# Optimization experiments

Hardware: AMD Instinct MI355X
Metric: run time of the kernel (lower is better)

Reference implementation:

```python
import jax, jax.numpy as jnp
import numpy as np

K = 3
PAD = 1
KP = K * K


def setup_inputs() -> dict:
    key = jax.random.key(0)
    k1, k2, k3, k4 = jax.random.split(key, 4)
    B, C, O, H, W = 8, 64, 64, 128, 128
    x = jax.random.normal(k1, (B, C, H, W), dtype=jnp.float32)
    offset = jax.random.normal(k2, (B, 2 * KP, H, W), dtype=jnp.float32)
    weight = jax.random.normal(k3, (O, C, K, K), dtype=jnp.float32) * 0.05
    bias = jax.random.normal(k4, (O,), dtype=jnp.float32) * 0.05
    return {"x": x, "offset": offset, "weight": weight, "bias": bias}


def _deform_conv(x, offset, weight, bias):
    B, C, H, W = x.shape
    O = weight.shape[0]
    x_pad = jnp.pad(x, ((0, 0), (0, 0), (PAD, PAD), (PAD, PAD)))
    Hp, Wp = H + 2 * PAD, W + 2 * PAD
    dt = x.dtype

    # kernel-point grid, row-major (yy, xx) as in torch meshgrid 'ij'
    r = K // 2
    rng = jnp.arange(-r, r + 1, dtype=dt)
    ky = jnp.repeat(rng, K)          # [KP]
    kx = jnp.tile(rng, K)            # [KP]

    base_y = jnp.arange(H, dtype=dt) + PAD
    base_x = jnp.arange(W, dtype=dt) + PAD

    off = offset.reshape(B, KP, 2, H, W)
    # sample coords in padded-image space; grid_sample align_corners=True
    # normalization cancels exactly, so sample at (cy, cx) directly.
    cy = base_y[None, None, :, None] + ky[None, :, None, None] + off[:, :, 0]  # [B,KP,H,W]
    cx = base_x[None, None, None, :] + kx[None, :, None, None] + off[:, :, 1]

    y0 = jnp.floor(cy)
    x0 = jnp.floor(cx)
    wy1 = cy - y0
    wx1 = cx - x0
    wy0 = 1.0 - wy1
    wx0 = 1.0 - wx1

    flat = x_pad.reshape(B, C, Hp * Wp)

    def gather(yi, xi):
        # zeros padding: out-of-bounds corner pixels contribute 0
        valid = ((yi >= 0) & (yi <= Hp - 1) & (xi >= 0) & (xi <= Wp - 1)).astype(dt)
        yc = jnp.clip(yi, 0, Hp - 1).astype(jnp.int32)
        xc = jnp.clip(xi, 0, Wp - 1).astype(jnp.int32)
        idx = (yc * Wp + xc).reshape(B, 1, KP * H * W)
        g = jnp.take_along_axis(flat, jnp.broadcast_to(idx, (B, C, KP * H * W)), axis=2)
        g = g.reshape(B, C, KP, H, W)
        return g * valid[:, None]  # broadcast valid [B,1,KP,H,W]

    sampled = (wy0 * wx0)[:, None] * gather(y0, x0) \
            + (wy0 * wx1)[:, None] * gather(y0, x0 + 1) \
            + (wy1 * wx0)[:, None] * gather(y0 + 1, x0) \
            + (wy1 * wx1)[:, None] * gather(y0 + 1, x0 + 1)  # [B,C,KP,H,W]

    w3 = weight.reshape(O, C, KP)
    out = jnp.einsum('bcphw,ocp->bohw', sampled, w3) + bias[None, :, None, None]
    return out


def reference(x, offset, weight, bias):
    return _deform_conv(x, offset, weight, bias)
```

## Files before the change

kernel.cpp:

```cpp
#include <hip/hip_runtime.h>
#include <hip/hip_bf16.h>

#define BB 8
#define CC 64
#define OO 64
#define HH 128
#define WW 128
#define HP 130
#define WP 130
#define KP 9

typedef __attribute__((ext_vector_type(8))) short bf16x8;
typedef __attribute__((ext_vector_type(4))) float f32x4;
typedef __attribute__((ext_vector_type(4))) unsigned u32x4;

#define ROWB 16640u

static __device__ __forceinline__ unsigned short f2bf(float f) {
  unsigned u = __float_as_uint(f);
  unsigned r = u + 0x7fffu + ((u >> 16) & 1u);
  return (unsigned short)(r >> 16);
}
static __device__ __forceinline__ f32x4 unpk4(unsigned lo, unsigned hi) {
  f32x4 r;
  r.x = __uint_as_float(lo << 16);
  r.y = __uint_as_float(lo & 0xffff0000u);
  r.z = __uint_as_float(hi << 16);
  r.w = __uint_as_float(hi & 0xffff0000u);
  return r;
}

__global__ __launch_bounds__(256) void k_xpose(const float* __restrict__ x,
                                               unsigned short* __restrict__ xt) {
  __shared__ unsigned short tile[128][66];
  int wg0 = blockIdx.x;
  int wg = (wg0 & 7) * 128 + (wg0 >> 3);
  int h = wg & 127, b = wg >> 7;
  int t = threadIdx.x;
  int w = t & 127, chalf = t >> 7;
  const float* xp = x + ((size_t)(b * CC) * HH + h) * WW;
#pragma unroll 4
  for (int c2 = 0; c2 < 32; ++c2) {
    int c = c2 * 2 + chalf;
    float v = xp[(size_t)c * HH * WW + w];
    tile[w][c] = f2bf(v);
  }
  __syncthreads();
  int c = t & 63, w2 = t >> 6;
  unsigned short* xtb = xt + (size_t)b * HP * WP * CC;
#pragma unroll 4
  for (int w4 = 0; w4 < 32; ++w4) {
    int ww = w4 * 4 + w2;
    xtb[((size_t)(h + 1) * WP + (ww + 1)) * CC + c] = tile[ww][c];
  }
  if (t < 128) {
    int xx = (t >= 64) ? (WP - 1) : 0;
    xtb[((size_t)(h + 1) * WP + xx) * CC + (t & 63)] = 0;
  }
  if (h == 0) {
    for (int i = t; i < 2 * WP * CC; i += 256) {
      int top = (i < WP * CC);
      int rem = top ? i : i - WP * CC;
      size_t y = top ? 0 : (HP - 1);
      xtb[y * WP * CC + rem] = 0;
    }
  }
}

__global__ __launch_bounds__(256) void k_wfrag(const float* __restrict__ wsrc,
                                               unsigned short* __restrict__ wf) {
  int flat = blockIdx.x * 256 + threadIdx.x;
  int j = flat & 7;
  int lane = (flat >> 3) & 63;
  int nf = (flat >> 9) & 3;
  int ks = (flat >> 11) & 1;
  int p = flat >> 12;
  int c = ks * 32 + ((lane >> 4) * 8) + j;
  int o = nf * 16 + (lane & 15);
  wf[flat] = f2bf(wsrc[(size_t)(o * CC + c) * KP + p]);
}

__global__ __launch_bounds__(256) void k_deform_main(const float* __restrict__ offset,
                                                     const float* __restrict__ bias,
                                                     const unsigned short* __restrict__ xt,
                                                     const unsigned short* __restrict__ wf,
                                                     float* __restrict__ out) {
  __shared__ __align__(16) char lds[20992];
  int wg0 = blockIdx.x;
  int wgs = (wg0 & 7) * 256 + (wg0 >> 3);
  int tile = wgs & 1, h = (wgs >> 1) & 127, b = wgs >> 8;
  int w0 = tile * 64;
  int t = threadIdx.x, wave = t >> 6, lane = t & 63;

  char* S0 = lds;
  uint2* cw = reinterpret_cast<uint2*>(lds + 16384) + wave * 144;

#pragma unroll
  for (int it = 0; it < 3; ++it) {
    int pair = it * 64 + lane;
    if (pair < 144) {
      int p = pair >> 4, pxl = pair & 15;
      int px = wave * 16 + pxl;
      int w = w0 + px;
      const float* offp = offset + (((size_t)b * 18 + 2 * p) * HH + h) * WW + w;
      float offy = offp[0];
      float offx = offp[HH * WW];
      float cy = (float)(h + p / 3) + offy;
      float cx = (float)(w + p % 3) + offx;
      float y0f = floorf(cy), x0f = floorf(cx);
      float wy1 = cy - y0f, wx1 = cx - x0f;
      int iy0 = (int)y0f, ix0 = (int)x0f;
      int iy0c = min(max(iy0, 0), HP - 1);
      int iy1c = min(max(iy0 + 1, 0), HP - 1);
      int ix0c = min(max(ix0, 0), WP - 1);
      int ix1c = min(max(ix0 + 1, 0), WP - 1);
      unsigned w0p = (unsigned)((iy0c * WP + ix0c) * (CC * 2));
      if (ix1c != ix0c) w0p |= (1u << 30);
      if (iy1c != iy0c) w0p |= (1u << 31);
      unsigned hv;
      asm("v_cvt_pkrtz_f16_f32 %0, %1, %2" : "=v"(hv) : "v"(wy1), "v"(wx1));
      uint2 ce;
      ce.x = w0p;
      ce.y = hv;
      cw[pair] = ce;
    }
  }

  f32x4 acc[4];
#pragma unroll
  for (int m = 0; m < 4; ++m) acc[m] = (f32x4){0.f, 0.f, 0.f, 0.f};

  const char* xb = (const char*)(xt + (size_t)b * HP * WP * CC);
  int c8 = lane & 7, pg = lane >> 3;
  unsigned cb = (unsigned)c8 * 16;
  unsigned swz = cb ^ ((unsigned)pg << 4);
  const uint2* cwl = cw + pg;

#define GLOADX(dst, voff) \
  asm volatile("global_load_dwordx4 %0, %1, %2" \
               : "=v"(dst) : "v"(voff), "s"(xb) : "memory")
#define GLOADW(dst, voff) \
  asm volatile("global_load_dwordx4 %0, %1, %2" \
               : "=v"(dst) : "v"(voff), "s"(wf) : "memory")

  auto LOADC = [&](int p, uint2* eo) {
#pragma unroll
    for (int it = 0; it < 2; ++it) eo[it] = cwl[p * 16 + it * 8];
  };
  auto ISSUE = [&](const uint2* ei, u32x4* go) {
#pragma unroll
    for (int it = 0; it < 2; ++it) {
      unsigned w0p = ei[it].x;
      unsigned a00 = (w0p & 0x003FFFFFu) + cb;
      unsigned dx = ((w0p >> 30) & 1u) << 7;
      unsigned dy = (w0p & 0x80000000u) ? ROWB : 0u;
      unsigned a01 = a00 + dx, a10 = a00 + dy, a11 = a10 + dx;
      GLOADX(go[it * 4 + 0], a00);
      GLOADX(go[it * 4 + 1], a01);
      GLOADX(go[it * 4 + 2], a10);
      GLOADX(go[it * 4 + 3], a11);
    }
  };
  auto BUILD = [&](const uint2* ei, const u32x4* gi, char* Sc) {
    char* swave = Sc + wave * 2048 + pg * 128;
#pragma unroll
    for (int it = 0; it < 2; ++it) {
      unsigned w1p = ei[it].y, w1hi = w1p >> 16;
      float wy1, wx1;
      asm("v_cvt_f32_f16 %0, %1" : "=v"(wy1) : "v"(w1p));
      asm("v_cvt_f32_f16 %0, %1" : "=v"(wx1) : "v"(w1hi));
      u32x4 q00 = gi[it * 4 + 0], q01 = gi[it * 4 + 1];
      u32x4 q10 = gi[it * 4 + 2], q11 = gi[it * 4 + 3];
      f32x4 a00 = unpk4(q00.x, q00.y), a01 = unpk4(q01.x, q01.y);
      f32x4 a10 = unpk4(q10.x, q10.y), a11 = unpk4(q11.x, q11.y);
      f32x4 topA = a00 + wx1 * (a01 - a00);
      f32x4 botA = a10 + wx1 * (a11 - a10);
      f32x4 sA = topA + wy1 * (botA - topA);
      f32x4 b00 = unpk4(q00.z, q00.w), b01 = unpk4(q01.z, q01.w);
      f32x4 b10 = unpk4(q10.z, q10.w), b11 = unpk4(q11.z, q11.w);
      f32x4 topB = b00 + wx1 * (b01 - b00);
      f32x4 botB = b10 + wx1 * (b11 - b10);
      f32x4 sB = topB + wy1 * (botB - topB);
      unsigned r0, r1, r2, r3;
      asm("v_cvt_pk_bf16_f32 %0, %1, %2" : "=v"(r0) : "v"(sA.x), "v"(sA.y));
      asm("v_cvt_pk_bf16_f32 %0, %1, %2" : "=v"(r1) : "v"(sA.z), "v"(sA.w));
      asm("v_cvt_pk_bf16_f32 %0, %1, %2" : "=v"(r2) : "v"(sB.x), "v"(sB.y));
      asm("v_cvt_pk_bf16_f32 %0, %1, %2" : "=v"(r3) : "v"(sB.z), "v"(sB.w));
      u32x4 pk; pk.x = r0; pk.y = r1; pk.z = r2; pk.w = r3;
      *reinterpret_cast<u32x4*>(swave + it * 1024 + swz) = pk;
    }
  };
  auto MFMA = [&](const char* Sc, bf16x8 b0, bf16x8 b1) {
    int l15 = lane & 15, kc = (lane >> 4) * 16, sw = (lane & 7) << 4;
#pragma unroll
    for (int m = 0; m < 4; ++m) {
      int rb = (m * 16 + l15) * 128;
      bf16x8 a0 = *reinterpret_cast<const bf16x8*>(Sc + rb + (kc ^ sw));
      bf16x8 a1 = *reinterpret_cast<const bf16x8*>(Sc + rb + ((64 + kc) ^ sw));
      acc[m] = __builtin_amdgcn_mfma_f32_16x16x32_bf16(a0, b0, acc[m], 0, 0, 0);
      acc[m] = __builtin_amdgcn_mfma_f32_16x16x32_bf16(a1, b1, acc[m], 0, 0, 0);
    }
  };

  uint2 e[2];
  u32x4 g[8];
  LOADC(0, e);
  ISSUE(e, g);
#pragma unroll
  for (int p = 0; p < 9; ++p) {
    char* Sc = S0 + (p & 1) * 8192;
    bf16x8 bv0, bv1;
    unsigned wfo = (unsigned)((p * 8 + wave) * 1024 + lane * 16);
    GLOADW(bv0, wfo);
    GLOADW(bv1, wfo + 4096);
    asm volatile("s_waitcnt vmcnt(2)" ::: "memory");
    __builtin_amdgcn_sched_barrier(0);
    BUILD(e, g, Sc);
    if (p < 8) LOADC(p + 1, e);
    asm volatile("s_waitcnt lgkmcnt(0)" ::: "memory");
    __builtin_amdgcn_s_barrier();
    if (p < 8) {
      ISSUE(e, g);
      asm volatile("s_waitcnt vmcnt(8)" ::: "memory");
    } else {
      asm volatile("s_waitcnt vmcnt(0)" ::: "memory");
    }
    __builtin_amdgcn_sched_barrier(0);
    MFMA(Sc, bv0, bv1);
  }
#undef GLOADX
#undef GLOADW

  __syncthreads();
  float* S2 = reinterpret_cast<float*>(lds);
  int l15 = lane & 15;
#pragma unroll
  for (int m = 0; m < 4; ++m) {
#pragma unroll
    for (int i2 = 0; i2 < 4; ++i2) {
      int px = m * 16 + ((lane >> 4) * 4) + i2;
      int o = wave * 16 + l15;
      S2[px * 65 + o] = acc[m][i2];
    }
  }
  __syncthreads();
  {
    int px = t & 63, o2 = t >> 6;
    float* op = out + (((size_t)b * OO) * HH + h) * WW + w0 + px;
#pragma unroll
    for (int o4 = 0; o4 < 16; ++o4) {
      int o = o4 * 4 + o2;
      op[(size_t)o * HH * WW] = S2[px * 65 + o] + bias[o];
    }
  }
}

extern "C" void kernel_launch(void* const* d_in, const int* in_sizes, int n_in,
                              void* d_out, int out_size, void* d_ws, size_t ws_size,
                              hipStream_t stream) {
  const float* x = (const float*)d_in[0];
  const float* offset = (const float*)d_in[1];
  const float* weight = (const float*)d_in[2];
  const float* bias = (const float*)d_in[3];
  float* out = (float*)d_out;

  unsigned short* xt = (unsigned short*)d_ws;
  unsigned short* wf = (unsigned short*)((char*)d_ws + 17305600);

  k_xpose<<<BB * HH, 256, 0, stream>>>(x, xt);
  k_wfrag<<<144, 256, 0, stream>>>(weight, wf);
  k_deform_main<<<BB * HH * 2, 256, 0, stream>>>(offset, bias, xt, wf, out);
}
```

Before: 53.61 us.

## Deepen gather prefetch to two stages and prefetch weights one step ahead

Double-buffers the coordinate/corner-gather registers so gathers for kernel point p+2 are issued while p is being built, and loads the MFMA weight fragments one iteration ahead. This hides more global-load latency behind the build and MFMA work. The bilinear interpolation is also rewritten as four weighted corner products instead of nested lerps. The cost is higher register pressure from the doubled buffers, which may reduce occupancy, and the vmcnt counts have to be tracked by hand.

After: 53.48 us. No clear change (-0.2%).

```diff
diff --git a/kernel.cpp b/kernel.cpp
--- a/kernel.cpp
+++ b/kernel.cpp
@@ -169,18 +169,18 @@
       float wy1, wx1;
       asm("v_cvt_f32_f16 %0, %1" : "=v"(wy1) : "v"(w1p));
       asm("v_cvt_f32_f16 %0, %1" : "=v"(wx1) : "v"(w1hi));
+      float w11 = wy1 * wx1;
+      float w01 = wx1 - w11;
+      float w10 = wy1 - w11;
+      float w00 = 1.0f - wx1 - w10;
       u32x4 q00 = gi[it * 4 + 0], q01 = gi[it * 4 + 1];
       u32x4 q10 = gi[it * 4 + 2], q11 = gi[it * 4 + 3];
       f32x4 a00 = unpk4(q00.x, q00.y), a01 = unpk4(q01.x, q01.y);
       f32x4 a10 = unpk4(q10.x, q10.y), a11 = unpk4(q11.x, q11.y);
-      f32x4 topA = a00 + wx1 * (a01 - a00);
-      f32x4 botA = a10 + wx1 * (a11 - a10);
-      f32x4 sA = topA + wy1 * (botA - topA);
+      f32x4 sA = w00 * a00 + w01 * a01 + w10 * a10 + w11 * a11;
       f32x4 b00 = unpk4(q00.z, q00.w), b01 = unpk4(q01.z, q01.w);
       f32x4 b10 = unpk4(q10.z, q10.w), b11 = unpk4(q11.z, q11.w);
-      f32x4 topB = b00 + wx1 * (b01 - b00);
-      f32x4 botB = b10 + wx1 * (b11 - b10);
-      f32x4 sB = topB + wy1 * (botB - topB);
+      f32x4 sB = w00 * b00 + w01 * b01 + w10 * b10 + w11 * b11;
       unsigned r0, r1, r2, r3;
       asm("v_cvt_pk_bf16_f32 %0, %1, %2" : "=v"(r0) : "v"(sA.x), "v"(sA.y));
       asm("v_cvt_pk_bf16_f32 %0, %1, %2" : "=v"(r1) : "v"(sA.z), "v"(sA.w));
@@ -202,31 +202,50 @@
     }
   };
 
-  uint2 e[2];
-  u32x4 g[8];
-  LOADC(0, e);
-  ISSUE(e, g);
+  uint2 eA[2], eB[2];
+  u32x4 gA[8], gB[8];
+  bf16x8 bvA0, bvA1, bvB0, bvB1;
+  LOADC(0, eA);
+  ISSUE(eA, gA);
+  {
+    unsigned wfo = (unsigned)((0 * 8 + wave) * 1024 + lane * 16);
+    GLOADW(bvA0, wfo);
+    GLOADW(bvA1, wfo + 4096);
+  }
+  LOADC(1, eB);
+  ISSUE(eB, gB);
+
 #pragma unroll
   for (int p = 0; p < 9; ++p) {
     char* Sc = S0 + (p & 1) * 8192;
-    bf16x8 bv0, bv1;
-    unsigned wfo = (unsigned)((p * 8 + wave) * 1024 + lane * 16);
-    GLOADW(bv0, wfo);
-    GLOADW(bv1, wfo + 4096);
-    asm volatile("s_waitcnt vmcnt(2)" ::: "memory");
+    uint2* eCur = (p & 1) ? eB : eA;
+    u32x4* gCur = (p & 1) ? gB : gA;
+    if (p < 8) {
+      asm volatile("s_waitcnt vmcnt(10)" ::: "memory");
+    } else {
+      asm volatile("s_waitcnt vmcnt(2)" ::: "memory");
+    }
     __builtin_amdgcn_sched_barrier(0);
-    BUILD(e, g, Sc);
-    if (p < 8) LOADC(p + 1, e);
+    BUILD(eCur, gCur, Sc);
+    if (p < 7) LOADC(p + 2, eCur);
     asm volatile("s_waitcnt lgkmcnt(0)" ::: "memory");
     __builtin_amdgcn_s_barrier();
     if (p < 8) {
-      ISSUE(e, g);
-      asm volatile("s_waitcnt vmcnt(8)" ::: "memory");
+      unsigned wfo = (unsigned)(((p + 1) * 8 + wave) * 1024 + lane * 16);
+      if (p & 1) { GLOADW(bvA0, wfo); GLOADW(bvA1, wfo + 4096); }
+      else       { GLOADW(bvB0, wfo); GLOADW(bvB1, wfo + 4096); }
+    }
+    if (p < 7) ISSUE(eCur, gCur);
+    if (p < 7) {
+      asm volatile("s_waitcnt vmcnt(18)" ::: "memory");
+    } else if (p == 7) {
+      asm volatile("s_waitcnt vmcnt(10)" ::: "memory");
     } else {
       asm volatile("s_waitcnt vmcnt(0)" ::: "memory");
     }
     __builtin_amdgcn_sched_barrier(0);
-    MFMA(Sc, bv0, bv1);
+    if (p & 1) MFMA(Sc, bvB0, bvB1);
+    else       MFMA(Sc, bvA0, bvA1);
   }
 #undef GLOADX
 #undef GLOADW
```
